# Optimization experiments

Measured on AMD Instinct MI355X. Metric: run time of the kernel, lower is better.

The kernel has to match this reference:

```python
import jax, jax.numpy as jnp
import numpy as np

N_EMBD = 768
N_HEAD = 12
EPS = 1e-5

def setup_inputs() -> dict:
    key = jax.random.key(0)
    ks = jax.random.split(key, 13)
    C = N_EMBD
    s = lambda n: 1.0 / np.sqrt(n)
    return {
        "x":      jax.random.normal(ks[0], (2, 2048, C), dtype=jnp.float32),
        "ln1_w":  jnp.ones((C,), jnp.float32),
        "ln1_b":  jnp.zeros((C,), jnp.float32),
        "w_qkv":  jax.random.normal(ks[1], (C, 3 * C), dtype=jnp.float32) * s(C),
        "b_qkv":  jnp.zeros((3 * C,), jnp.float32),
        "w_proj": jax.random.normal(ks[2], (C, C), dtype=jnp.float32) * s(C),
        "b_proj": jnp.zeros((C,), jnp.float32),
        "ln2_w":  jnp.ones((C,), jnp.float32),
        "ln2_b":  jnp.zeros((C,), jnp.float32),
        "w_fc1":  jax.random.normal(ks[3], (C, 4 * C), dtype=jnp.float32) * s(C),
        "b_fc1":  jnp.zeros((4 * C,), jnp.float32),
        "w_fc2":  jax.random.normal(ks[4], (4 * C, C), dtype=jnp.float32) * s(4 * C),
        "b_fc2":  jnp.zeros((C,), jnp.float32),
    }

def _layernorm(x, w, b):
    mu = jnp.mean(x, axis=-1, keepdims=True)
    var = jnp.mean(jnp.square(x - mu), axis=-1, keepdims=True)
    return (x - mu) * jax.lax.rsqrt(var + EPS) * w + b

def reference(x, ln1_w, ln1_b, w_qkv, b_qkv, w_proj, b_proj,
              ln2_w, ln2_b, w_fc1, b_fc1, w_fc2, b_fc2):
    B, T, C = x.shape
    H = N_HEAD
    hd = C // H
    # --- attention branch ---
    h = _layernorm(x, ln1_w, ln1_b)
    qkv = h @ w_qkv + b_qkv                                  # [B,T,3C]
    q, k, v = jnp.split(qkv, 3, axis=-1)
    q = q.reshape(B, T, H, hd).transpose(0, 2, 1, 3)          # [B,H,T,hd]
    k = k.reshape(B, T, H, hd).transpose(0, 2, 1, 3)
    v = v.reshape(B, T, H, hd).transpose(0, 2, 1, 3)
    att = jnp.einsum('bhqd,bhkd->bhqk', q, k) * (1.0 / np.sqrt(hd))
    causal = jnp.tril(jnp.ones((T, T), dtype=bool))
    att = jnp.where(causal, att, -jnp.inf)
    att = jax.nn.softmax(att, axis=-1)
    y = jnp.einsum('bhqk,bhkd->bhqd', att, v)                 # [B,H,T,hd]
    y = y.transpose(0, 2, 1, 3).reshape(B, T, C)
    x = x + (y @ w_proj + b_proj)
    # --- MLP branch (dropout = identity in eval) ---
    h = _layernorm(x, ln2_w, ln2_b)
    h = jax.nn.gelu(h @ w_fc1 + b_fc1, approximate=False)
    x = x + (h @ w_fc2 + b_fc2)
    return x
```

## Files before the change

kernel.cpp:

```cpp
#include <hip/hip_runtime.h>
#include <math.h>

typedef __attribute__((ext_vector_type(8))) short short8;
typedef __attribute__((ext_vector_type(4))) float floatx4;

__device__ __forceinline__ unsigned short f2bf(float f) {
    union { float f; unsigned u; } v; v.f = f;
    unsigned r = v.u + 0x7fffu + ((v.u >> 16) & 1u);
    return (unsigned short)(r >> 16);
}

__device__ __forceinline__ unsigned short f2bf_t(float f) {
    union { float f; unsigned u; } v; v.f = f;
    return (unsigned short)(v.u >> 16);
}

__device__ __forceinline__ float bf2f(unsigned short h) {
    union { unsigned u; float f; } v; v.u = ((unsigned)h) << 16; return v.f;
}

__device__ __forceinline__ float fexp2(float x) {
#if __has_builtin(__builtin_amdgcn_exp2f)
    return __builtin_amdgcn_exp2f(x);
#else
    return __expf(x * 0.69314718056f);
#endif
}

__device__ __forceinline__ void gload16(const unsigned short* g, unsigned short* l) {
    __builtin_amdgcn_global_load_lds(
        (const __attribute__((address_space(1))) unsigned int*)g,
        (__attribute__((address_space(3))) unsigned int*)l, 16, 0, 0);
}

__global__ __launch_bounds__(256) void ln_kernel(const float* __restrict__ x,
                                                 const float* __restrict__ w,
                                                 const float* __restrict__ b,
                                                 unsigned short* __restrict__ o) {
    int row = blockIdx.x, tid = threadIdx.x;
    const float* xr = x + (size_t)row * 768;
    float v0 = xr[tid], v1 = xr[tid + 256], v2 = xr[tid + 512];
    float s = v0 + v1 + v2, ss = v0 * v0 + v1 * v1 + v2 * v2;
#pragma unroll
    for (int o_ = 32; o_; o_ >>= 1) { s += __shfl_xor(s, o_); ss += __shfl_xor(ss, o_); }
    __shared__ float red[8];
    if ((tid & 63) == 0) { red[tid >> 6] = s; red[(tid >> 6) + 4] = ss; }
    __syncthreads();
    s = red[0] + red[1] + red[2] + red[3];
    ss = red[4] + red[5] + red[6] + red[7];
    float mu = s * (1.f / 768.f);
    float var = ss * (1.f / 768.f) - mu * mu;
    float inv = rsqrtf(var + 1e-5f);
    unsigned short* orow = o + (size_t)row * 768;
    orow[tid]       = f2bf((v0 - mu) * inv * w[tid]       + b[tid]);
    orow[tid + 256] = f2bf((v1 - mu) * inv * w[tid + 256] + b[tid + 256]);
    orow[tid + 512] = f2bf((v2 - mu) * inv * w[tid + 512] + b[tid + 512]);
}

__global__ __launch_bounds__(256) void wt_all_kernel(
    const float* __restrict__ w0, unsigned short* __restrict__ t0,
    const float* __restrict__ w1, unsigned short* __restrict__ t1,
    const float* __restrict__ w2, unsigned short* __restrict__ t2,
    const float* __restrict__ w3, unsigned short* __restrict__ t3) {
    int bid = (int)blockIdx.x;
    const float* w; unsigned short* wt; int K, N, bx, by;
    if (bid < 1728)      { w = w0; wt = t0; K = 768;  N = 2304; int l = bid;        bx = l % 72; by = l / 72; }
    else if (bid < 2304) { w = w1; wt = t1; K = 768;  N = 768;  int l = bid - 1728; bx = l % 24; by = l / 24; }
    else if (bid < 4608) { w = w2; wt = t2; K = 768;  N = 3072; int l = bid - 2304; bx = l % 96; by = l / 96; }
    else                 { w = w3; wt = t3; K = 3072; N = 768;  int l = bid - 4608; bx = l % 24; by = l / 24; }
    __shared__ float t[32][33];
    int n0 = bx * 32, k0 = by * 32;
    int tx = threadIdx.x & 31, ty = threadIdx.x >> 5;
#pragma unroll
    for (int i = 0; i < 32; i += 8)
        t[ty + i][tx] = w[(size_t)(k0 + ty + i) * N + n0 + tx];
    __syncthreads();
#pragma unroll
    for (int i = 0; i < 32; i += 8)
        wt[(size_t)(n0 + ty + i) * K + k0 + tx] = f2bf(t[tx][ty + i]);
}

template <int EPI>
__global__ __launch_bounds__(256) void gemm_kernel(
    const unsigned short* __restrict__ A, const unsigned short* __restrict__ Bt,
    const float* __restrict__ bias, const float* __restrict__ resid,
    float* __restrict__ fout, unsigned short* __restrict__ o0,
    unsigned short* __restrict__ o1, unsigned short* __restrict__ o2,
    int K, int Kcnt) {
    __shared__ unsigned short Al[2][128 * 32];
    __shared__ unsigned short Bl[2][128 * 32];
    int tid = threadIdx.x, lane = tid & 63, w = tid >> 6;
    int wm = w >> 1, wn = w & 1;
    int nwg = (int)(gridDim.x * gridDim.y);
    int wgid = (int)(blockIdx.y * gridDim.x + blockIdx.x);
    int logical = (wgid & 7) * (nwg >> 3) + (wgid >> 3);
    int by = logical & 31, bx = logical >> 5;
    int m0 = by * 128;
    int n0, kof = 0, chunk = 0;
    if (EPI == 4) {
        n0 = (bx % 6) * 128;
        chunk = bx / 6;
        kof = chunk * Kcnt;
    } else {
        n0 = bx * 128;
    }
    int lr = lane & 15, lk = (lane >> 4) << 3;

    int srow = w * 32 + (lane >> 2);
    int sko = (lane & 3) << 3;
    const unsigned short* Ab = A + (size_t)(m0 + srow) * K + kof + sko;
    const unsigned short* Bb = Bt + (size_t)(n0 + srow) * K + kof + sko;

    floatx4 acc[4][4];
#pragma unroll
    for (int i = 0; i < 4; i++)
#pragma unroll
        for (int j = 0; j < 4; j++) acc[i][j] = (floatx4){0.f, 0.f, 0.f, 0.f};

    int nk = Kcnt >> 5;
    auto stage = [&](int buf, int t) {
        int k0 = t << 5;
        unsigned short* Alp = &Al[buf][(w * 32) * 32];
        unsigned short* Blp = &Bl[buf][(w * 32) * 32];
        gload16(Ab + k0, Alp);
        gload16(Ab + 16 * K + k0, Alp + 16 * 32);
        gload16(Bb + k0, Blp);
        gload16(Bb + 16 * K + k0, Blp + 16 * 32);
    };

    stage(0, 0);
    for (int t = 0; t < nk; t++) {
        int cur = t & 1;
        __syncthreads();
        if (t + 1 < nk) stage(cur ^ 1, t + 1);
        short8 af[4], bfr[4];
#pragma unroll
        for (int mt = 0; mt < 4; mt++) af[mt] = *(short8*)&Al[cur][(wm * 64 + mt * 16 + lr) * 32 + lk];
#pragma unroll
        for (int nt = 0; nt < 4; nt++) bfr[nt] = *(short8*)&Bl[cur][(wn * 64 + nt * 16 + lr) * 32 + lk];
#pragma unroll
        for (int mt = 0; mt < 4; mt++)
#pragma unroll
            for (int nt = 0; nt < 4; nt++)
                acc[mt][nt] = __builtin_amdgcn_mfma_f32_16x16x32_bf16(af[mt], bfr[nt], acc[mt][nt], 0, 0, 0);
    }

    int mb = m0 + wm * 64, nb = n0 + wn * 64;
    int sec = 0;
    if (EPI == 0) sec = n0 / 768;
#pragma unroll
    for (int mt = 0; mt < 4; mt++)
#pragma unroll
        for (int nt = 0; nt < 4; nt++)
#pragma unroll
            for (int r = 0; r < 4; r++) {
                int mrow = mb + mt * 16 + ((lane >> 4) << 2) + r;
                int ncol = nb + nt * 16 + lr;
                float val = acc[mt][nt][r];
                if (EPI != 4) val += bias[ncol];
                if (EPI == 0) {
                    int f = ncol - sec * 768;
                    int h = f >> 6, d = f & 63;
                    int bb = mrow >> 11, t = mrow & 2047;
                    if (sec == 0)
                        o0[((size_t)(bb * 12 + h) * 2048 + t) * 64 + d] = f2bf(val * 0.1803368801f);
                    else if (sec == 1)
                        o1[((size_t)(bb * 12 + h) * 2048 + t) * 64 + d] = f2bf(val);
                    else
                        o2[((size_t)(bb * 12 + h) * 64 + d) * 2048 + t] = f2bf(val);
                } else if (EPI == 1) {
                    fout[(size_t)mrow * 768 + ncol] = val + resid[(size_t)mrow * 768 + ncol];
                } else if (EPI == 2) {
                    float g = 0.5f * val * (1.f + erff(val * 0.70710678118f));
                    o0[(size_t)mrow * 3072 + ncol] = f2bf(g);
                } else if (EPI == 4) {
                    unsigned short* op = (chunk == 0) ? o0 : (chunk == 1) ? o1
                                       : (chunk == 2) ? o2 : (unsigned short*)fout;
                    op[(size_t)mrow * 768 + ncol] = f2bf(val);
                }
            }
}

__global__ __launch_bounds__(256) void sk_combine(
    const unsigned short* __restrict__ p0, const unsigned short* __restrict__ p1,
    const unsigned short* __restrict__ p2, const unsigned short* __restrict__ p3,
    const float* __restrict__ bias, const float* __restrict__ resid,
    float* __restrict__ out) {
    int i = blockIdx.x * 256 + threadIdx.x;
    size_t base = (size_t)i * 8;
    int col = (int)(base % 768);
    short8 a0 = *(const short8*)&p0[base];
    short8 a1 = *(const short8*)&p1[base];
    short8 a2 = *(const short8*)&p2[base];
    short8 a3 = *(const short8*)&p3[base];
#pragma unroll
    for (int j = 0; j < 8; j++) {
        float s = bf2f((unsigned short)a0[j]) + bf2f((unsigned short)a1[j]) +
                  bf2f((unsigned short)a2[j]) + bf2f((unsigned short)a3[j]);
        out[base + j] = s + bias[col + j] + resid[base + j];
    }
}

__global__ __launch_bounds__(256) void attn_kernel(const unsigned short* __restrict__ q_s,
                                                   const unsigned short* __restrict__ k_s,
                                                   const unsigned short* __restrict__ v_t,
                                                   unsigned short* __restrict__ y,
                                                   unsigned short* __restrict__ opart,
                                                   float* __restrict__ lpart) {
    __shared__ unsigned short KVs[2][4096];
    __shared__ unsigned short Pls[4][32][72];
    const int T = 2048, H = 12;
    int tid = threadIdx.x, lane = tid & 63, w = tid >> 6;
    int xx = (int)blockIdx.x;
    int bq, c;
    if (xx < 16)      { c = 0; bq = xx; }
    else if (xx < 28) { c = 1; bq = xx - 12; }
    else if (xx < 36) { c = 2; bq = xx - 20; }
    else              { c = 3; bq = xx - 24; }
    int bh = blockIdx.y;
    int bi = bh / H, hh = bh - bi * H;
    const unsigned short* qp = q_s + (size_t)bh * T * 64;
    const unsigned short* kp = k_s + (size_t)bh * T * 64;
    const unsigned short* vp = v_t + (size_t)bh * 64 * T;
    int wq0 = bq * 128 + w * 32;
    int lr = lane & 15, lk8 = (lane >> 4) << 3, hi = lane >> 4;
    int nt_blk = 2 * bq + 2;
    int t0 = c * 8;
    int t1 = t0 + 8 < nt_blk ? t0 + 8 : nt_blk;

    unsigned short (*Pl)[72] = Pls[w];
    int srow = tid >> 3, ssl = tid & 7;

    auto stage = [&](int buf, int t) {
        int kv0 = t * 64;
        unsigned short* base = &KVs[buf][(tid >> 6) * 512];
#pragma unroll
        for (int h = 0; h < 2; h++) {
            int r = srow + h * 32;
            int ss = ssl ^ (r & 7);
            gload16(kp + (size_t)(kv0 + r) * 64 + ss * 8, base + h * 2048);
        }
    };

    short8 aq[2][2];
#pragma unroll
    for (int mt = 0; mt < 2; mt++)
#pragma unroll
        for (int kf = 0; kf < 2; kf++)
            aq[mt][kf] = *(const short8*)&qp[(size_t)(wq0 + mt * 16 + lr) * 64 + kf * 32 + lk8];

    floatx4 yacc[2][4];
    float lacc[2][4];
#pragma unroll
    for (int i = 0; i < 2; i++)
#pragma unroll
        for (int j = 0; j < 4; j++) {
            yacc[i][j] = (floatx4){0.f, 0.f, 0.f, 0.f};
            lacc[i][j] = 0.f;
        }

    stage(0, t0);
    __syncthreads();

    for (int t = t0; t < t1; t++) {
        int cur = (t - t0) & 1;
        if (t + 1 < t1) stage(cur ^ 1, t + 1);
        int kv0 = t * 64;
        if (kv0 <= wq0 + 31) {
            const unsigned short* Kt = &KVs[cur][0];
            floatx4 sacc[2][4];
#pragma unroll
            for (int i = 0; i < 2; i++)
#pragma unroll
                for (int j = 0; j < 4; j++) sacc[i][j] = (floatx4){0.f, 0.f, 0.f, 0.f};
#pragma unroll
            for (int kf = 0; kf < 2; kf++) {
                int sl = ((kf << 2) | hi) ^ (lr & 7);
                short8 bk[4];
#pragma unroll
                for (int nt = 0; nt < 4; nt++)
                    bk[nt] = *(const short8*)&Kt[(nt * 16 + lr) * 64 + sl * 8];
#pragma unroll
                for (int mt = 0; mt < 2; mt++)
#pragma unroll
                    for (int nt = 0; nt < 4; nt++)
                        sacc[mt][nt] = __builtin_amdgcn_mfma_f32_16x16x32_bf16(aq[mt][kf], bk[nt], sacc[mt][nt], 0, 0, 0);
            }
            short8 bv[4][2];
#pragma unroll
            for (int nt = 0; nt < 4; nt++)
#pragma unroll
                for (int kf = 0; kf < 2; kf++)
                    bv[nt][kf] = *(const short8*)&vp[(size_t)(nt * 16 + lr) * T + kv0 + kf * 32 + lk8];
            bool full = (kv0 + 63 <= wq0);
#pragma unroll
            for (int mt = 0; mt < 2; mt++)
#pragma unroll
                for (int r = 0; r < 4; r++) {
                    int qg = wq0 + mt * 16 + (hi << 2) + r;
                    int prow = mt * 16 + (hi << 2) + r;
#pragma unroll
                    for (int nt = 0; nt < 4; nt++) {
                        float sv = sacc[mt][nt][r];
                        if (!full) {
                            int kvg = kv0 + nt * 16 + lr;
                            sv = (kvg <= qg) ? sv : -1e30f;
                        }
                        float p = fexp2(sv);
                        lacc[mt][r] += p;
                        Pl[prow][nt * 16 + lr] = f2bf_t(p);
                    }
                }
#pragma unroll
            for (int kf = 0; kf < 2; kf++) {
                short8 pa[2];
#pragma unroll
                for (int mt = 0; mt < 2; mt++) pa[mt] = *(short8*)&Pl[mt * 16 + lr][kf * 32 + lk8];
#pragma unroll
                for (int mt = 0; mt < 2; mt++)
#pragma unroll
                    for (int nt = 0; nt < 4; nt++)
                        yacc[mt][nt] = __builtin_amdgcn_mfma_f32_16x16x32_bf16(pa[mt], bv[nt][kf], yacc[mt][nt], 0, 0, 0);
            }
        }
        __syncthreads();
    }

    if (bq < 4) {
#pragma unroll
        for (int mt = 0; mt < 2; mt++)
#pragma unroll
            for (int r = 0; r < 4; r++) {
                float l = lacc[mt][r];
                l += __shfl_xor(l, 1);
                l += __shfl_xor(l, 2);
                l += __shfl_xor(l, 4);
                l += __shfl_xor(l, 8);
                float inv = 1.f / l;
                int qg = wq0 + mt * 16 + (hi << 2) + r;
#pragma unroll
                for (int nt = 0; nt < 4; nt++)
                    y[((size_t)(bi * T + qg)) * 768 + hh * 64 + nt * 16 + lr] = f2bf(yacc[mt][nt][r] * inv);
            }
    } else {
        int g = bq >> 2, rr = bq & 3;
        int base = (g == 1) ? 2 * rr : (g == 2) ? 8 + 3 * rr : 20 + 4 * rr;
        int slab = bh * 36 + base + c;
        unsigned short* op = opart + (size_t)slab * 8192;
        float* lp = lpart + (size_t)slab * 128;
#pragma unroll
        for (int mt = 0; mt < 2; mt++)
#pragma unroll
            for (int r = 0; r < 4; r++) {
                float l = lacc[mt][r];
                l += __shfl_xor(l, 1);
                l += __shfl_xor(l, 2);
                l += __shfl_xor(l, 4);
                l += __shfl_xor(l, 8);
                int wrow = w * 32 + mt * 16 + (hi << 2) + r;
                if (lr == 0) lp[wrow] = l;
#pragma unroll
                for (int nt = 0; nt < 4; nt++)
                    op[(size_t)wrow * 64 + nt * 16 + lr] = f2bf(yacc[mt][nt][r]);
            }
    }
}

__global__ __launch_bounds__(256) void attn_combine(const unsigned short* __restrict__ opart,
                                                    const float* __restrict__ lpart,
                                                    unsigned short* __restrict__ y) {
    const int T = 2048, H = 12;
    int bq = 4 + (int)blockIdx.x;
    int bh = blockIdx.y;
    int bi = bh / H, hh = bh - bi * H;
    int nchunk = (bq >> 2) + 1;
    int g = bq >> 2, rr = bq & 3;
    int base = (g == 1) ? 2 * rr : (g == 2) ? 8 + 3 * rr : 20 + 4 * rr;
    int tid = threadIdx.x;
    int row = tid >> 1, cb = (tid & 1) * 32;

    float l = 0.f;
    for (int c = 0; c < nchunk; c++) l += lpart[(size_t)(bh * 36 + base + c) * 128 + row];
    float inv = 1.f / l;

    float s[32];
#pragma unroll
    for (int j = 0; j < 32; j++) s[j] = 0.f;
    for (int c = 0; c < nchunk; c++) {
        const unsigned short* op = opart + ((size_t)(bh * 36 + base + c) * 128 + row) * 64 + cb;
#pragma unroll
        for (int v = 0; v < 4; v++) {
            short8 ob = *(const short8*)&op[v * 8];
#pragma unroll
            for (int j = 0; j < 8; j++) s[v * 8 + j] += bf2f((unsigned short)ob[j]);
        }
    }
    int qg = bq * 128 + row;
    unsigned short* yr = y + ((size_t)(bi * T + qg)) * 768 + hh * 64 + cb;
#pragma unroll
    for (int v = 0; v < 4; v++) {
        short8 ob;
#pragma unroll
        for (int j = 0; j < 8; j++) ob[j] = (short)f2bf(s[v * 8 + j] * inv);
        *(short8*)&yr[v * 8] = ob;
    }
}

extern "C" void kernel_launch(void* const* d_in, const int* in_sizes, int n_in,
                              void* d_out, int out_size, void* d_ws, size_t ws_size,
                              hipStream_t stream) {
    const float* x    = (const float*)d_in[0];
    const float* ln1w = (const float*)d_in[1];
    const float* ln1b = (const float*)d_in[2];
    const float* wqkv = (const float*)d_in[3];
    const float* bqkv = (const float*)d_in[4];
    const float* wproj= (const float*)d_in[5];
    const float* bproj= (const float*)d_in[6];
    const float* ln2w = (const float*)d_in[7];
    const float* ln2b = (const float*)d_in[8];
    const float* wfc1 = (const float*)d_in[9];
    const float* bfc1 = (const float*)d_in[10];
    const float* wfc2 = (const float*)d_in[11];
    const float* bfc2 = (const float*)d_in[12];
    float* out = (float*)d_out;

    char* ws = (char*)d_ws;
    size_t off = 0;
    auto alloc = [&](size_t bytes) { void* p = ws + off; off += (bytes + 255) & ~(size_t)255; return p; };

    const size_t MT = 4096;
    unsigned short* wqkv_t = (unsigned short*)alloc(2304 * 768 * 2);
    unsigned short* wproj_t= (unsigned short*)alloc(768 * 768 * 2);
    unsigned short* wfc1_t = (unsigned short*)alloc(3072 * 768 * 2);
    unsigned short* wfc2_t = (unsigned short*)alloc(768 * 3072 * 2);
    unsigned short* h12    = (unsigned short*)alloc(MT * 768 * 2);
    float*          x1     = (float*)alloc(MT * 768 * 4);
    unsigned short* qs     = (unsigned short*)alloc(MT * 768 * 2);
    unsigned short* ks     = (unsigned short*)alloc(MT * 768 * 2);
    unsigned short* vt     = (unsigned short*)alloc(MT * 768 * 2);
    unsigned short* yb     = (unsigned short*)alloc(MT * 768 * 2);
    unsigned short* hm     = qs;
    unsigned short* opart  = (unsigned short*)alloc(24 * 36 * 8192 * 2);
    float*          lpart  = (float*)alloc(24 * 36 * 128 * 4);

    unsigned short* p0 = (unsigned short*)ws;
    unsigned short* p1 = opart;
    unsigned short* p2 = (unsigned short*)((char*)opart + (size_t)MT * 768 * 2);
    unsigned short* p3 = h12;

    wt_all_kernel<<<dim3(6912), 256, 0, stream>>>(wqkv, wqkv_t, wproj, wproj_t,
                                                  wfc1, wfc1_t, wfc2, wfc2_t);

    ln_kernel<<<4096, 256, 0, stream>>>(x, ln1w, ln1b, h12);
    gemm_kernel<0><<<dim3(18, 32), 256, 0, stream>>>(h12, wqkv_t, bqkv, nullptr, nullptr, qs, ks, vt, 768, 768);
    attn_kernel<<<dim3(40, 24), 256, 0, stream>>>(qs, ks, vt, yb, opart, lpart);
    attn_combine<<<dim3(12, 24), 256, 0, stream>>>(opart, lpart, yb);
    gemm_kernel<1><<<dim3(6, 32), 256, 0, stream>>>(yb, wproj_t, bproj, x, x1, nullptr, nullptr, nullptr, 768, 768);
    ln_kernel<<<4096, 256, 0, stream>>>(x1, ln2w, ln2b, h12);
    gemm_kernel<2><<<dim3(24, 32), 256, 0, stream>>>(h12, wfc1_t, bfc1, nullptr, nullptr, hm, nullptr, nullptr, 768, 768);
    gemm_kernel<4><<<dim3(24, 32), 256, 0, stream>>>(hm, wfc2_t, nullptr, nullptr, (float*)p3, p0, p1, p2, 3072, 768);
    sk_combine<<<dim3(1536), 256, 0, stream>>>(p0, p1, p2, p3, bfc2, x1, out);
}
```

Before: 212.0 us.

## Halve attention query tile to 64 rows with 2-wave blocks and more splits

Shrinks each attention block from 128 query rows on 4 waves to 64 query rows on 2 waves. The grid doubles to 80x24 and the split-KV partial-slab layout is remapped to 72 slabs per head, each holding 64 rows. The combine kernel is adjusted to match. The aim is finer work granularity and less causal-masking waste on diagonal tiles, at the cost of staging each K/V tile once per 64 query rows instead of once per 128.

```diff
diff --git a/kernel.cpp b/kernel.cpp
--- a/kernel.cpp
+++ b/kernel.cpp
@@ -201,44 +201,43 @@
     }
 }
 
-__global__ __launch_bounds__(256) void attn_kernel(const unsigned short* __restrict__ q_s,
+__global__ __launch_bounds__(128) void attn_kernel(const unsigned short* __restrict__ q_s,
                                                    const unsigned short* __restrict__ k_s,
                                                    const unsigned short* __restrict__ v_t,
                                                    unsigned short* __restrict__ y,
                                                    unsigned short* __restrict__ opart,
                                                    float* __restrict__ lpart) {
     __shared__ unsigned short KVs[2][4096];
-    __shared__ unsigned short Pls[4][32][72];
+    __shared__ unsigned short Pls[2][32][72];
     const int T = 2048, H = 12;
     int tid = threadIdx.x, lane = tid & 63, w = tid >> 6;
     int xx = (int)blockIdx.x;
-    int bq, c;
-    if (xx < 16)      { c = 0; bq = xx; }
-    else if (xx < 28) { c = 1; bq = xx - 12; }
-    else if (xx < 36) { c = 2; bq = xx - 20; }
-    else              { c = 3; bq = xx - 24; }
+    int qb, c;
+    if (xx < 32)      { c = 0; qb = xx; }
+    else if (xx < 56) { c = 1; qb = xx - 24; }
+    else if (xx < 72) { c = 2; qb = xx - 40; }
+    else              { c = 3; qb = xx - 48; }
     int bh = blockIdx.y;
     int bi = bh / H, hh = bh - bi * H;
     const unsigned short* qp = q_s + (size_t)bh * T * 64;
     const unsigned short* kp = k_s + (size_t)bh * T * 64;
     const unsigned short* vp = v_t + (size_t)bh * 64 * T;
-    int wq0 = bq * 128 + w * 32;
+    int wq0 = qb * 64 + w * 32;
     int lr = lane & 15, lk8 = (lane >> 4) << 3, hi = lane >> 4;
-    int nt_blk = 2 * bq + 2;
+    int nt_blk = qb + 1;
     int t0 = c * 8;
     int t1 = t0 + 8 < nt_blk ? t0 + 8 : nt_blk;
 
     unsigned short (*Pl)[72] = Pls[w];
-    int srow = tid >> 3, ssl = tid & 7;
 
     auto stage = [&](int buf, int t) {
         int kv0 = t * 64;
-        unsigned short* base = &KVs[buf][(tid >> 6) * 512];
-#pragma unroll
-        for (int h = 0; h < 2; h++) {
-            int r = srow + h * 32;
-            int ss = ssl ^ (r & 7);
-            gload16(kp + (size_t)(kv0 + r) * 64 + ss * 8, base + h * 2048);
+        unsigned short* base = &KVs[buf][w * 512];
+#pragma unroll
+        for (int h = 0; h < 4; h++) {
+            int r = w * 8 + h * 16 + (lane >> 3);
+            int ss = (lane & 7) ^ (r & 7);
+            gload16(kp + (size_t)(kv0 + r) * 64 + ss * 8, base + h * 1024);
         }
     };
 
@@ -326,7 +325,7 @@
         __syncthreads();
     }
 
-    if (bq < 4) {
+    if (nt_blk <= 8) {
 #pragma unroll
         for (int mt = 0; mt < 2; mt++)
 #pragma unroll
@@ -343,11 +342,12 @@
                     y[((size_t)(bi * T + qg)) * 768 + hh * 64 + nt * 16 + lr] = f2bf(yacc[mt][nt][r] * inv);
             }
     } else {
-        int g = bq >> 2, rr = bq & 3;
-        int base = (g == 1) ? 2 * rr : (g == 2) ? 8 + 3 * rr : 20 + 4 * rr;
-        int slab = bh * 36 + base + c;
-        unsigned short* op = opart + (size_t)slab * 8192;
-        float* lp = lpart + (size_t)slab * 128;
+        int base = (qb <= 15) ? (qb - 8) * 2
+                 : (qb <= 23) ? 16 + (qb - 16) * 3
+                              : 40 + (qb - 24) * 4;
+        int slab = bh * 72 + base + c;
+        unsigned short* op = opart + (size_t)slab * 4096;
+        float* lp = lpart + (size_t)slab * 64;
 #pragma unroll
         for (int mt = 0; mt < 2; mt++)
 #pragma unroll
@@ -370,35 +370,36 @@
                                                     const float* __restrict__ lpart,
                                                     unsigned short* __restrict__ y) {
     const int T = 2048, H = 12;
-    int bq = 4 + (int)blockIdx.x;
+    int qb = 8 + (int)blockIdx.x;
     int bh = blockIdx.y;
     int bi = bh / H, hh = bh - bi * H;
-    int nchunk = (bq >> 2) + 1;
-    int g = bq >> 2, rr = bq & 3;
-    int base = (g == 1) ? 2 * rr : (g == 2) ? 8 + 3 * rr : 20 + 4 * rr;
+    int nchunk = (qb <= 15) ? 2 : (qb <= 23) ? 3 : 4;
+    int base = (qb <= 15) ? (qb - 8) * 2
+             : (qb <= 23) ? 16 + (qb - 16) * 3
+                          : 40 + (qb - 24) * 4;
     int tid = threadIdx.x;
-    int row = tid >> 1, cb = (tid & 1) * 32;
+    int row = tid >> 2, cb = (tid & 3) * 16;
 
     float l = 0.f;
-    for (int c = 0; c < nchunk; c++) l += lpart[(size_t)(bh * 36 + base + c) * 128 + row];
+    for (int c = 0; c < nchunk; c++) l += lpart[(size_t)(bh * 72 + base + c) * 64 + row];
     float inv = 1.f / l;
 
-    float s[32];
-#pragma unroll
-    for (int j = 0; j < 32; j++) s[j] = 0.f;
+    float s[16];
+#pragma unroll
+    for (int j = 0; j < 16; j++) s[j] = 0.f;
     for (int c = 0; c < nchunk; c++) {
-        const unsigned short* op = opart + ((size_t)(bh * 36 + base + c) * 128 + row) * 64 + cb;
-#pragma unroll
-        for (int v = 0; v < 4; v++) {
+        const unsigned short* op = opart + ((size_t)(bh * 72 + base + c) * 64 + row) * 64 + cb;
+#pragma unroll
+        for (int v = 0; v < 2; v++) {
             short8 ob = *(const short8*)&op[v * 8];
 #pragma unroll
             for (int j = 0; j < 8; j++) s[v * 8 + j] += bf2f((unsigned short)ob[j]);
         }
     }
-    int qg = bq * 128 + row;
+    int qg = qb * 64 + row;
     unsigned short* yr = y + ((size_t)(bi * T + qg)) * 768 + hh * 64 + cb;
 #pragma unroll
-    for (int v = 0; v < 4; v++) {
+    for (int v = 0; v < 2; v++) {
         short8 ob;
 #pragma unroll
         for (int j = 0; j < 8; j++) ob[j] = (short)f2bf(s[v * 8 + j] * inv);
@@ -440,8 +441,8 @@
     unsigned short* vt     = (unsigned short*)alloc(MT * 768 * 2);
     unsigned short* yb     = (unsigned short*)alloc(MT * 768 * 2);
     unsigned short* hm     = qs;
-    unsigned short* opart  = (unsigned short*)alloc(24 * 36 * 8192 * 2);
-    float*          lpart  = (float*)alloc(24 * 36 * 128 * 4);
+    unsigned short* opart  = (unsigned short*)alloc((size_t)24 * 72 * 4096 * 2);
+    float*          lpart  = (float*)alloc((size_t)24 * 72 * 64 * 4);
 
     unsigned short* p0 = (unsigned short*)ws;
     unsigned short* p1 = opart;
@@ -453,8 +454,8 @@
 
     ln_kernel<<<4096, 256, 0, stream>>>(x, ln1w, ln1b, h12);
     gemm_kernel<0><<<dim3(18, 32), 256, 0, stream>>>(h12, wqkv_t, bqkv, nullptr, nullptr, qs, ks, vt, 768, 768);
-    attn_kernel<<<dim3(40, 24), 256, 0, stream>>>(qs, ks, vt, yb, opart, lpart);
-    attn_combine<<<dim3(12, 24), 256, 0, stream>>>(opart, lpart, yb);
+    attn_kernel<<<dim3(80, 24), 128, 0, stream>>>(qs, ks, vt, yb, opart, lpart);
+    attn_combine<<<dim3(24, 24), 256, 0, stream>>>(opart, lpart, yb);
     gemm_kernel<1><<<dim3(6, 32), 256, 0, stream>>>(yb, wproj_t, bproj, x, x1, nullptr, nullptr, nullptr, 768, 768);
     ln_kernel<<<4096, 256, 0, stream>>>(x1, ln2w, ln2b, h12);
     gemm_kernel<2><<<dim3(24, 32), 256, 0, stream>>>(h12, wfc1_t, bfc1, nullptr, nullptr, hm, nullptr, nullptr, 768, 768);
```

Measured after the change: 206.4 us. -2.6%, faster.
